# Performance work log

Hardware: AMD Instinct MI355X
Metric: run time of the kernel (lower is better)

Reference implementation:

```python
import jax, jax.numpy as jnp
import numpy as np

B, NH, WH, WW, C, NPOS = 64, 16, 16, 16, 64, 288
N = WH * WW


def setup_inputs() -> dict:
    key = jax.random.key(0)
    k1, k2, k3 = jax.random.split(key, 3)
    query = jax.random.normal(k1, (B, NH, N, C), dtype=jnp.float32)
    attn_logits = jax.random.normal(k2, (B, NH, N, N), dtype=jnp.float32)
    pos_emb = jax.random.normal(k3, (C, NPOS), dtype=jnp.float32) * 0.02
    return {"query": query, "attn_logits": attn_logits, "pos_emb": pos_emb,
            "Wh": WH, "Ww": WW, "npos_max": NPOS}


def _rev_cumsum(x):
    # flip -> cumsum -> flip along last axis
    return jnp.flip(jnp.cumsum(jnp.flip(x, -1), axis=-1), -1)


def reference(query, attn_logits, pos_emb, Wh, Ww, npos_max):
    B_, nH, N_, C_ = query.shape
    gates = jax.nn.sigmoid(attn_logits)                       # (B,nH,N,N)
    gates_h = gates.swapaxes(-1, -2).reshape(B_, nH, N_, Ww, Wh)
    gates_w = gates.reshape(B_, nH, N_, Wh, Ww)
    pos_h = _rev_cumsum(gates_h).reshape(B_, nH, N_, N_).swapaxes(-1, -2)
    pos_w = _rev_cumsum(gates_w).reshape(B_, nH, N_, N_)
    pos = pos_h * Ww + pos_w
    pos = jnp.minimum(pos, npos_max - 1)
    pos_floor = jnp.floor(pos)
    pos_ceil_i = jnp.ceil(pos).astype(jnp.int32)
    pos_floor_i = pos_floor.astype(jnp.int32)
    # (B,nH,N,C) @ (C,npos) -> (B,nH,N,npos)
    logits_int = jnp.einsum('bhnc,cp->bhnp', query, pos_emb)
    logits_ceil = jnp.take_along_axis(logits_int, pos_ceil_i, axis=-1)
    logits_floor = jnp.take_along_axis(logits_int, pos_floor_i, axis=-1)
    w = pos - pos_floor
    return logits_ceil * w + logits_floor * (1.0 - w)
```

## Files before the change

kernel.cpp:

```cpp
#include <hip/hip_runtime.h>


#define NPOS 288
#define NT   18
#define LTS2 292

typedef __attribute__((ext_vector_type(8))) short bf16x8;
typedef __attribute__((ext_vector_type(4))) float f32x4;

__device__ __forceinline__ unsigned short f2bf(float f) {
    unsigned u = __float_as_uint(f);
    u += 0x7FFF + ((u >> 16) & 1);
    return (unsigned short)(u >> 16);
}
__device__ __forceinline__ float bf2f(unsigned short b) {
    return __uint_as_float(((unsigned)b) << 16);
}

template <int D>
__device__ __forceinline__ float suffix_step(float v) {
    int s = __builtin_amdgcn_update_dpp(0, __float_as_int(v), 0x100 | D, 0xF, 0xF, true);
    return v + __int_as_float(s);
}

__global__ void prep_kernel(const float* __restrict__ pos_emb,
                            short* __restrict__ wsb) {
    int idx = blockIdx.x * blockDim.x + threadIdx.x;
    if (idx >= NT * 2 * 64) return;
    int l = idx & 63;
    int s = (idx >> 6) & 1;
    int t = idx >> 7;
    int col = t * 16 + (l & 15);
    int k0  = s * 32 + (l >> 4) * 8;
    short* dst = wsb + idx * 8;
    #pragma unroll
    for (int j = 0; j < 8; ++j)
        dst[j] = (short)f2bf(pos_emb[(k0 + j) * NPOS + col]);
}

__global__ __launch_bounds__(256, 4) void cope2d_kernel(
    const float* __restrict__ query,
    const float* __restrict__ attn_logits,
    const bf16x8* __restrict__ wsb8,
    float* __restrict__ out)
{
    __shared__ unsigned short Lb[16 * LTS2];

    const int tid  = threadIdx.x;
    const int lane = tid & 63;
    const int wave = tid >> 6;
    const int blk  = blockIdx.x;
    const int bh   = blk >> 2;
    const int p0   = (blk & 3) * 4;

    long rowbase = (long)bh * 256 + p0 * 16;
    long gb      = rowbase * 256;

    const float* qp = query + (rowbase + (lane & 15)) * 64 + (lane >> 4) * 8;
    f32x4 q00 = *(const f32x4*)(qp);
    f32x4 q01 = *(const f32x4*)(qp + 4);
    f32x4 q10 = *(const f32x4*)(qp + 32);
    f32x4 q11 = *(const f32x4*)(qp + 36);
    float gn[16];
    #pragma unroll
    for (int i = 0; i < 16; ++i)
        gn[i] = attn_logits[gb + (long)i * 256 + tid];

    for (int s = 0; s < 4; ++s) {
        bf16x8 A0, A1;
        #pragma unroll
        for (int j = 0; j < 4; ++j) {
            A0[j]     = (short)f2bf(q00[j]);
            A0[4 + j] = (short)f2bf(q01[j]);
            A1[j]     = (short)f2bf(q10[j]);
            A1[4 + j] = (short)f2bf(q11[j]);
        }

        if (s) __syncthreads();

        for (int t = wave; t < NT; t += 4) {
            f32x4 c = {0.f, 0.f, 0.f, 0.f};
            c = __builtin_amdgcn_mfma_f32_16x16x32_bf16(A0, wsb8[(t * 2 + 0) * 64 + lane], c, 0, 0, 0);
            c = __builtin_amdgcn_mfma_f32_16x16x32_bf16(A1, wsb8[(t * 2 + 1) * 64 + lane], c, 0, 0, 0);
            const int col = t * 16 + (lane & 15);
            const int r0  = (lane >> 4) * 4;
            #pragma unroll
            for (int r = 0; r < 4; ++r)
                Lb[(r0 + r) * LTS2 + col] = f2bf(c[r]);
        }

        float g[16];
        #pragma unroll
        for (int i = 0; i < 16; ++i)
            g[i] = 1.0f / (1.0f + __expf(-gn[i]));

        __syncthreads();

        const long gbs = gb;

        if (s < 3) {
            rowbase += 16;
            gb = rowbase * 256;
            const float* qp2 = query + (rowbase + (lane & 15)) * 64 + (lane >> 4) * 8;
            q00 = *(const f32x4*)(qp2);
            q01 = *(const f32x4*)(qp2 + 4);
            q10 = *(const f32x4*)(qp2 + 32);
            q11 = *(const f32x4*)(qp2 + 36);
            #pragma unroll
            for (int i = 0; i < 16; ++i)
                gn[i] = attn_logits[gb + (long)i * 256 + tid];
        }

        float run = 0.f;
        #pragma unroll
        for (int half = 1; half >= 0; --half) {
            const int i0 = half * 8;
            float r8[8];
            #pragma unroll
            for (int k = 7; k >= 0; --k) { run += g[i0 + k]; r8[k] = run; }

            float w8[8]; int fi8[8];
            #pragma unroll
            for (int k = 0; k < 8; ++k) {
                float pw = suffix_step<8>(suffix_step<4>(suffix_step<2>(suffix_step<1>(g[i0 + k]))));
                float pos = fminf(r8[k] * 16.0f + pw, 287.0f);
                float pf = floorf(pos);
                fi8[k] = (int)pf;
                w8[k]  = pos - pf;
            }
            float lf8[8], lc8[8];
            #pragma unroll
            for (int k = 0; k < 8; ++k) {
                const unsigned short* Lr = Lb + (i0 + k) * LTS2;
                lf8[k] = bf2f(Lr[fi8[k]]);
                lc8[k] = bf2f(Lr[fi8[k] + 1]);
            }
            #pragma unroll
            for (int k = 0; k < 8; ++k)
                out[gbs + (long)(i0 + k) * 256 + tid] =
                    lf8[k] + w8[k] * (lc8[k] - lf8[k]);
        }
    }
}

extern "C" void kernel_launch(void* const* d_in, const int* in_sizes, int n_in,
                              void* d_out, int out_size, void* d_ws, size_t ws_size,
                              hipStream_t stream) {
    const float* query       = (const float*)d_in[0];
    const float* attn_logits = (const float*)d_in[1];
    const float* pos_emb     = (const float*)d_in[2];
    float* outp = (float*)d_out;
    short* wsb  = (short*)d_ws;

    prep_kernel<<<9, 256, 0, stream>>>(pos_emb, wsb);
    cope2d_kernel<<<4096, 256, 0, stream>>>(query, attn_logits,
                                            (const bf16x8*)d_ws, outp);
}
```

Baseline: 139.9 us.

## Double-buffer LDS logits tile, pack bf16 conversions, raise occupancy hint

Splits the shared logits tile into two buffers alternated by stage parity, so the barrier at the top of each stage can be dropped and one stage's MFMA writes can overlap the previous stage's reads. Query conversion now uses the packed v_cvt_pk_bf16_f32 instruction instead of manual rounding. Launch bounds go from 4 to 8 blocks per CU, and 64-bit index arithmetic becomes 32-bit pointer increments to save address instructions. The tighter register budget could cause spills, and the doubled LDS (about 18 KB per block) may limit how many blocks fit per CU.

```diff
diff --git a/kernel.cpp b/kernel.cpp
--- a/kernel.cpp
+++ b/kernel.cpp
@@ -15,6 +15,11 @@
 }
 __device__ __forceinline__ float bf2f(unsigned short b) {
     return __uint_as_float(((unsigned)b) << 16);
+}
+__device__ __forceinline__ unsigned cvt_pk_bf16(float lo, float hi) {
+    unsigned r;
+    asm("v_cvt_pk_bf16_f32 %0, %1, %2" : "=v"(r) : "v"(lo), "v"(hi));
+    return r;
 }
 
 template <int D>
@@ -38,13 +43,13 @@
         dst[j] = (short)f2bf(pos_emb[(k0 + j) * NPOS + col]);
 }
 
-__global__ __launch_bounds__(256, 4) void cope2d_kernel(
+__global__ __launch_bounds__(256, 8) void cope2d_kernel(
     const float* __restrict__ query,
     const float* __restrict__ attn_logits,
     const bf16x8* __restrict__ wsb8,
     float* __restrict__ out)
 {
-    __shared__ unsigned short Lb[16 * LTS2];
+    __shared__ unsigned short Lb[2][16 * LTS2];
 
     const int tid  = threadIdx.x;
     const int lane = tid & 63;
@@ -53,40 +58,43 @@
     const int bh   = blk >> 2;
     const int p0   = (blk & 3) * 4;
 
-    long rowbase = (long)bh * 256 + p0 * 16;
-    long gb      = rowbase * 256;
+    int rowbase = bh * 256 + p0 * 16;
+    int gb      = rowbase * 256;
 
-    const float* qp = query + (rowbase + (lane & 15)) * 64 + (lane >> 4) * 8;
+    const float* qp = query + rowbase * 64 + (lane & 15) * 64 + (lane >> 4) * 8;
     f32x4 q00 = *(const f32x4*)(qp);
     f32x4 q01 = *(const f32x4*)(qp + 4);
     f32x4 q10 = *(const f32x4*)(qp + 32);
     f32x4 q11 = *(const f32x4*)(qp + 36);
     float gn[16];
-    #pragma unroll
-    for (int i = 0; i < 16; ++i)
-        gn[i] = attn_logits[gb + (long)i * 256 + tid];
+    {
+        const float* gp = attn_logits + gb + tid;
+        #pragma unroll
+        for (int i = 0; i < 16; ++i)
+            gn[i] = gp[i * 256];
+    }
 
     for (int s = 0; s < 4; ++s) {
-        bf16x8 A0, A1;
-        #pragma unroll
-        for (int j = 0; j < 4; ++j) {
-            A0[j]     = (short)f2bf(q00[j]);
-            A0[4 + j] = (short)f2bf(q01[j]);
-            A1[j]     = (short)f2bf(q10[j]);
-            A1[4 + j] = (short)f2bf(q11[j]);
-        }
+        union { bf16x8 v; unsigned u[4]; } A0, A1;
+        A0.u[0] = cvt_pk_bf16(q00[0], q00[1]);
+        A0.u[1] = cvt_pk_bf16(q00[2], q00[3]);
+        A0.u[2] = cvt_pk_bf16(q01[0], q01[1]);
+        A0.u[3] = cvt_pk_bf16(q01[2], q01[3]);
+        A1.u[0] = cvt_pk_bf16(q10[0], q10[1]);
+        A1.u[1] = cvt_pk_bf16(q10[2], q10[3]);
+        A1.u[2] = cvt_pk_bf16(q11[0], q11[1]);
+        A1.u[3] = cvt_pk_bf16(q11[2], q11[3]);
 
-        if (s) __syncthreads();
-
+        unsigned short* Lbs = Lb[s & 1];
         for (int t = wave; t < NT; t += 4) {
             f32x4 c = {0.f, 0.f, 0.f, 0.f};
-            c = __builtin_amdgcn_mfma_f32_16x16x32_bf16(A0, wsb8[(t * 2 + 0) * 64 + lane], c, 0, 0, 0);
-            c = __builtin_amdgcn_mfma_f32_16x16x32_bf16(A1, wsb8[(t * 2 + 1) * 64 + lane], c, 0, 0, 0);
+            c = __builtin_amdgcn_mfma_f32_16x16x32_bf16(A0.v, wsb8[(t * 2 + 0) * 64 + lane], c, 0, 0, 0);
+            c = __builtin_amdgcn_mfma_f32_16x16x32_bf16(A1.v, wsb8[(t * 2 + 1) * 64 + lane], c, 0, 0, 0);
             const int col = t * 16 + (lane & 15);
             const int r0  = (lane >> 4) * 4;
             #pragma unroll
             for (int r = 0; r < 4; ++r)
-                Lb[(r0 + r) * LTS2 + col] = f2bf(c[r]);
+                Lbs[(r0 + r) * LTS2 + col] = f2bf(c[r]);
         }
 
         float g[16];
@@ -94,23 +102,25 @@
         for (int i = 0; i < 16; ++i)
             g[i] = 1.0f / (1.0f + __expf(-gn[i]));
 
+        const int gout = gb;
+
         __syncthreads();
-
-        const long gbs = gb;
 
         if (s < 3) {
             rowbase += 16;
-            gb = rowbase * 256;
-            const float* qp2 = query + (rowbase + (lane & 15)) * 64 + (lane >> 4) * 8;
+            gb += 16 * 256;
+            const float* qp2 = query + rowbase * 64 + (lane & 15) * 64 + (lane >> 4) * 8;
             q00 = *(const f32x4*)(qp2);
             q01 = *(const f32x4*)(qp2 + 4);
             q10 = *(const f32x4*)(qp2 + 32);
             q11 = *(const f32x4*)(qp2 + 36);
+            const float* gp2 = attn_logits + gb + tid;
             #pragma unroll
             for (int i = 0; i < 16; ++i)
-                gn[i] = attn_logits[gb + (long)i * 256 + tid];
+                gn[i] = gp2[i * 256];
         }
 
+        float* op = out + gout + tid;
         float run = 0.f;
         #pragma unroll
         for (int half = 1; half >= 0; --half) {
@@ -131,14 +141,13 @@
             float lf8[8], lc8[8];
             #pragma unroll
             for (int k = 0; k < 8; ++k) {
-                const unsigned short* Lr = Lb + (i0 + k) * LTS2;
+                const unsigned short* Lr = Lbs + (i0 + k) * LTS2;
                 lf8[k] = bf2f(Lr[fi8[k]]);
                 lc8[k] = bf2f(Lr[fi8[k] + 1]);
             }
             #pragma unroll
             for (int k = 0; k < 8; ++k)
-                out[gbs + (long)(i0 + k) * 256 + tid] =
-                    lf8[k] + w8[k] * (lc8[k] - lf8[k]);
+                op[(i0 + k) * 256] = lf8[k] + w8[k] * (lc8[k] - lf8[k]);
         }
     }
 }
```

New measurement: 203.7 us. +45.6%, slower.
